# Kernel tuning notes

Hardware: AMD Instinct MI355X
Metric: run time of the kernel (lower is better)

The kernel has to match this reference:

```python
import jax, jax.numpy as jnp
import numpy as np

GAMMA = 1.0 / 512.0  # RBF bandwidth, 1/d_feat


def _rbf_kernel(X, Z, gamma):
    # X: [N, d], Z: [M, d] -> K: [N, M], K[i,j] = exp(-gamma * ||x_i - z_j||^2)
    xn = jnp.sum(X * X, axis=1, keepdims=True)        # [N, 1]
    zn = jnp.sum(Z * Z, axis=1, keepdims=True).T      # [1, M]
    sq = xn + zn - 2.0 * (X @ Z.T)                    # [N, M]
    return jnp.exp(-gamma * jnp.maximum(sq, 0.0))


def setup_inputs() -> dict:
    key = jax.random.key(0)
    k1, k2, k3, k4, k5 = jax.random.split(key, 5)
    N, d, M = 8192, 512, 4096
    inputs = jax.random.normal(k1, (M, d), dtype=jnp.float32)
    X = jax.random.normal(k2, (N, d), dtype=jnp.float32)
    # SVM labels in {-1, +1}
    Y = jnp.where(jax.random.uniform(k3, (N, 1)) > 0.5, 1.0, -1.0).astype(jnp.float32)
    a = jax.random.normal(k4, (N, 1), dtype=jnp.float32) * 0.1
    b = jax.random.normal(k5, (1, 1), dtype=jnp.float32)
    return {"inputs": inputs, "X": X, "Y": Y, "a": a, "b": b}


def reference(inputs, X, Y, a, b):
    # K: [N, M]; weighted sum over support vectors N, then add bias, transpose.
    K = _rbf_kernel(X, inputs, GAMMA)                 # [N, M]
    s = jnp.sum(a * Y * K, axis=0)                    # [M]
    out = (s + b)                                     # [1, M] via broadcast with [1,1]
    return out.T                                      # [M, 1]
```

## Files before the change

kernel.cpp:

```cpp
#include <hip/hip_runtime.h>
#include <hip/hip_bf16.h>
#include <stdint.h>

#define C2EXP (-0.0028179443441958f)

static constexpr int N_SV = 8192;
static constexpr int M_Q  = 4096;
static constexpr int DIM  = 512;
static constexpr int NP_A = N_SV / 16;
static constexpr int NP_B = M_Q / 16;
static constexpr int NKT  = DIM / 32;

typedef __bf16 bf16x8 __attribute__((ext_vector_type(8)));
typedef float  f32x4  __attribute__((ext_vector_type(4)));

#define GLB const __attribute__((address_space(1))) void
#define LDS __attribute__((address_space(3))) void

__global__ __launch_bounds__(256) void svm_prep(
    const float* __restrict__ Z, const float* __restrict__ X,
    const float* __restrict__ Y, const float* __restrict__ a,
    const float* __restrict__ b,
    __bf16* __restrict__ Xp, __bf16* __restrict__ Zp,
    float* __restrict__ xn, float* __restrict__ zn, float* __restrict__ w,
    float* __restrict__ out)
{
    __shared__ float part[4][16];

    const int tid  = threadIdx.x;
    const int lane = tid & 63;
    const int wv   = tid >> 6;
    const int pb   = blockIdx.x;
    const bool isA = (pb < NP_A);
    const int p    = isA ? pb : pb - NP_A;
    const float* src = (isA ? X : Z) + (size_t)p * 16 * DIM;
    __bf16* dst  = isA ? Xp : Zp;
    const int np = isA ? NP_A : NP_B;

    const int q    = p & 15;
    const int tile = p >> 4;
    const int slot = isA ? (((q >> 2) & 1) * 8 + (q >> 3) * 4 + (q & 3))
                         : (((q >> 1) & 1) * 8 + (q >> 2) * 2 + (q & 1));
    const size_t stIdx = (size_t)tile * 16 + slot;

    const int row = lane & 15;
    const int ch  = lane >> 4;

    float s = 0.0f;
    #pragma unroll
    for (int f = 0; f < 4; ++f) {
        const int kt = wv * 4 + f;
        const float4* rp = (const float4*)(src + (size_t)row * DIM + kt * 32 + ch * 8);
        float4 v0 = rp[0], v1 = rp[1];
        s += v0.x*v0.x + v0.y*v0.y + v0.z*v0.z + v0.w*v0.w
           + v1.x*v1.x + v1.y*v1.y + v1.z*v1.z + v1.w*v1.w;
        __bf16 h[8] = {(__bf16)v0.x, (__bf16)v0.y, (__bf16)v0.z, (__bf16)v0.w,
                       (__bf16)v1.x, (__bf16)v1.y, (__bf16)v1.z, (__bf16)v1.w};
        uint4 bits;
        __builtin_memcpy(&bits, h, 16);
        *(uint4*)((char*)dst + (((size_t)kt * np + stIdx) << 10) + lane * 16) = bits;
    }

    s += __shfl_xor(s, 16);
    s += __shfl_xor(s, 32);
    if (lane < 16) part[wv][lane] = s;
    __syncthreads();

    if (tid < 16) {
        const float t = part[0][tid] + part[1][tid] + part[2][tid] + part[3][tid];
        const int r = p * 16 + tid;
        if (isA) { xn[r] = t; w[r] = a[r] * Y[r]; }
        else     { zn[r] = t; out[r] = b[0]; }
    }
}

__global__ __launch_bounds__(512, 2) void svm_main(
    const __bf16* __restrict__ Xp, const __bf16* __restrict__ Zp,
    const float* __restrict__ xn, const float* __restrict__ zn,
    const float* __restrict__ w, float* __restrict__ out)
{
    __shared__ char Sh[65536];

    const int tid  = threadIdx.x;
    const int lane = tid & 63;
    const int wid  = tid >> 6;
    const int wr   = wid >> 2;
    const int wc   = wid & 3;

    const int iBase = blockIdx.y * 256;
    const int jBase = blockIdx.x * 256;
    const int pbA   = blockIdx.y * 16;
    const int pbB   = blockIdx.x * 16;

    f32x4 acc[8][4];
    #pragma unroll
    for (int m = 0; m < 8; ++m)
        #pragma unroll
        for (int n = 0; n < 4; ++n)
            acc[m][n] = (f32x4)(0.0f);

    auto stageH = [&](const __bf16* Mp, int pb16, int kt, int op, int h, int np) {
        char* dst = (char*)Sh + (kt & 1) * 32768 + op * 16384 + h * 8192 + tid * 16;
        const char* s0 = (const char*)Mp + (((size_t)kt * np + pb16) << 10)
                       + h * 8192 + tid * 16;
        __builtin_amdgcn_global_load_lds((GLB*)s0, (LDS*)dst, 16, 0, 0);
    };

    stageH(Xp, pbA, 0, 0, 0, NP_A);
    stageH(Xp, pbA, 0, 0, 1, NP_A);
    stageH(Zp, pbB, 0, 1, 0, NP_B);
    stageH(Zp, pbB, 0, 1, 1, NP_B);
    stageH(Xp, pbA, 1, 0, 0, NP_A);
    stageH(Xp, pbA, 1, 0, 1, NP_A);
    stageH(Zp, pbB, 1, 1, 0, NP_B);
    stageH(Zp, pbB, 1, 1, 1, NP_B);
    asm volatile("s_waitcnt vmcnt(4)" ::: "memory");
    __builtin_amdgcn_s_barrier();

    bf16x8 af[4], bf[4];

    #pragma unroll
    for (int t = 0; t < NKT; ++t) {
        const int buf = t & 1;
        const char* Ab = (const char*)Sh + buf * 32768 + lane * 16;
        const char* Bb = Ab + 16384;

        #pragma unroll
        for (int mi = 0; mi < 4; ++mi)
            af[mi] = *(const bf16x8*)(Ab + (wr * 4 + mi) * 1024);
        #pragma unroll
        for (int j = 0; j < 2; ++j)
            bf[j] = *(const bf16x8*)(Bb + (wc * 2 + j) * 1024);
        __builtin_amdgcn_s_barrier();
        asm volatile("s_waitcnt lgkmcnt(0)" ::: "memory");
        __builtin_amdgcn_sched_barrier(0);
        __builtin_amdgcn_s_setprio(1);
        #pragma unroll
        for (int mi = 0; mi < 4; ++mi)
            #pragma unroll
            for (int n = 0; n < 2; ++n)
                acc[mi][n] = __builtin_amdgcn_mfma_f32_16x16x32_bf16(
                    af[mi], bf[n], acc[mi][n], 0, 0, 0);
        __builtin_amdgcn_s_setprio(0);
        __builtin_amdgcn_s_barrier();

        #pragma unroll
        for (int j = 0; j < 2; ++j)
            bf[2 + j] = *(const bf16x8*)(Bb + (8 + wc * 2 + j) * 1024);
        if (t + 2 < NKT) {
            stageH(Xp, pbA, t + 2, 0, 0, NP_A);
            stageH(Zp, pbB, t + 2, 1, 0, NP_B);
        }
        __builtin_amdgcn_s_barrier();
        asm volatile("s_waitcnt lgkmcnt(0)" ::: "memory");
        __builtin_amdgcn_sched_barrier(0);
        __builtin_amdgcn_s_setprio(1);
        #pragma unroll
        for (int mi = 0; mi < 4; ++mi)
            #pragma unroll
            for (int n = 2; n < 4; ++n)
                acc[mi][n] = __builtin_amdgcn_mfma_f32_16x16x32_bf16(
                    af[mi], bf[n], acc[mi][n], 0, 0, 0);
        __builtin_amdgcn_s_setprio(0);
        __builtin_amdgcn_s_barrier();

        #pragma unroll
        for (int mi = 0; mi < 4; ++mi)
            af[mi] = *(const bf16x8*)(Ab + (8 + wr * 4 + mi) * 1024);
        if (t + 2 < NKT)
            stageH(Zp, pbB, t + 2, 1, 1, NP_B);
        __builtin_amdgcn_s_barrier();
        asm volatile("s_waitcnt lgkmcnt(0)" ::: "memory");
        __builtin_amdgcn_sched_barrier(0);
        __builtin_amdgcn_s_setprio(1);
        #pragma unroll
        for (int mi = 0; mi < 4; ++mi)
            #pragma unroll
            for (int n = 0; n < 2; ++n)
                acc[4 + mi][n] = __builtin_amdgcn_mfma_f32_16x16x32_bf16(
                    af[mi], bf[n], acc[4 + mi][n], 0, 0, 0);
        __builtin_amdgcn_s_setprio(0);
        __builtin_amdgcn_s_barrier();

        if (t + 2 < NKT)
            stageH(Xp, pbA, t + 2, 0, 1, NP_A);
        __builtin_amdgcn_s_barrier();
        asm volatile("s_waitcnt lgkmcnt(0)" ::: "memory");
        __builtin_amdgcn_sched_barrier(0);
        __builtin_amdgcn_s_setprio(1);
        #pragma unroll
        for (int mi = 0; mi < 4; ++mi)
            #pragma unroll
            for (int n = 2; n < 4; ++n)
                acc[4 + mi][n] = __builtin_amdgcn_mfma_f32_16x16x32_bf16(
                    af[mi], bf[n], acc[4 + mi][n], 0, 0, 0);
        __builtin_amdgcn_s_setprio(0);
        if (t < NKT - 2) {
            asm volatile("s_waitcnt vmcnt(4)" ::: "memory");
        } else if (t == NKT - 2) {
            asm volatile("s_waitcnt vmcnt(0)" ::: "memory");
        }
        __builtin_amdgcn_s_barrier();
    }

    const int rg   = lane >> 4;
    const int lcol = lane & 15;

    float znv[4];
    #pragma unroll
    for (int n = 0; n < 4; ++n)
        znv[n] = zn[jBase + wc * 64 + n * 16 + lcol];

    float cs[4] = {0.f, 0.f, 0.f, 0.f};
    #pragma unroll
    for (int m = 0; m < 8; ++m) {
        float wv[4], xv[4];
        #pragma unroll
        for (int r = 0; r < 4; ++r) {
            const int i = iBase + wr * 128 + m * 16 + rg * 4 + r;
            wv[r] = w[i];
            xv[r] = xn[i];
        }
        #pragma unroll
        for (int n = 0; n < 4; ++n)
            #pragma unroll
            for (int r = 0; r < 4; ++r) {
                float d = xv[r] + znv[n] - 2.0f * acc[m][n][r];
                d = fmaxf(d, 0.0f);
                cs[n] += wv[r] * exp2f(C2EXP * d);
            }
    }

    #pragma unroll
    for (int n = 0; n < 4; ++n) {
        const int j = jBase + wc * 64 + n * 16 + lcol;
        float c = cs[n];
        c += __shfl_xor(c, 16);
        c += __shfl_xor(c, 32);
        if (lane < 16) atomicAdd(out + j, c);
    }
}

extern "C" void kernel_launch(void* const* d_in, const int* in_sizes, int n_in,
                              void* d_out, int out_size, void* d_ws, size_t ws_size,
                              hipStream_t stream)
{
    const float* Z = (const float*)d_in[0];
    const float* X = (const float*)d_in[1];
    const float* Y = (const float*)d_in[2];
    const float* a = (const float*)d_in[3];
    const float* b = (const float*)d_in[4];
    float* out = (float*)d_out;

    char* ws = (char*)d_ws;
    __bf16* Xp = (__bf16*)ws;
    __bf16* Zp = (__bf16*)(ws + 8ull * 1024 * 1024);
    float*  xn = (float*)(ws + 12ull * 1024 * 1024);
    float*  zn = xn + N_SV;
    float*  w  = zn + M_Q;

    svm_prep<<<NP_A + NP_B, 256, 0, stream>>>(Z, X, Y, a, b, Xp, Zp, xn, zn, w, out);
    svm_main<<<dim3(M_Q / 256, N_SV / 256), 512, 0, stream>>>(Xp, Zp, xn, zn, w, out);
}
```

Measured before the change: 113.5 us.

## Restructure GEMM main loop into two phases with fewer barriers

Rewrites the K-loop schedule of the fused RBF GEMM. Each iteration now has two 16-MFMA phases instead of four 8-MFMA phases. The global-to-LDS staging is split into a one-load part issued one tile ahead and a three-load part issued two tiles ahead, with vmcnt waits adjusted to match. The goal is to cut barrier and waitcnt stalls per K-step and give each phase more MFMA work. In exchange, B fragments are held in more registers at once, and the reworked prefetch and wait ordering raises the risk of LDS races.

```diff
diff --git a/kernel.cpp b/kernel.cpp
--- a/kernel.cpp
+++ b/kernel.cpp
@@ -105,15 +105,18 @@
                        + h * 8192 + tid * 16;
         __builtin_amdgcn_global_load_lds((GLB*)s0, (LDS*)dst, 16, 0, 0);
     };
-
-    stageH(Xp, pbA, 0, 0, 0, NP_A);
-    stageH(Xp, pbA, 0, 0, 1, NP_A);
-    stageH(Zp, pbB, 0, 1, 0, NP_B);
-    stageH(Zp, pbB, 0, 1, 1, NP_B);
-    stageH(Xp, pbA, 1, 0, 0, NP_A);
-    stageH(Xp, pbA, 1, 0, 1, NP_A);
-    stageH(Zp, pbB, 1, 1, 0, NP_B);
-    stageH(Zp, pbB, 1, 1, 1, NP_B);
+    auto stage3 = [&](int kt) {
+        stageH(Xp, pbA, kt, 0, 0, NP_A);
+        stageH(Zp, pbB, kt, 1, 0, NP_B);
+        stageH(Zp, pbB, kt, 1, 1, NP_B);
+    };
+    auto stage1 = [&](int kt) {
+        stageH(Xp, pbA, kt, 0, 1, NP_A);
+    };
+
+    stage3(0);
+    stage1(0);
+    stage3(1);
     asm volatile("s_waitcnt vmcnt(4)" ::: "memory");
     __builtin_amdgcn_s_barrier();
 
@@ -121,86 +124,51 @@
 
     #pragma unroll
     for (int t = 0; t < NKT; ++t) {
-        const int buf = t & 1;
-        const char* Ab = (const char*)Sh + buf * 32768 + lane * 16;
+        const char* Ab = (const char*)Sh + (t & 1) * 32768 + lane * 16;
         const char* Bb = Ab + 16384;
 
+        if (t + 1 < NKT) stage1(t + 1);
         #pragma unroll
         for (int mi = 0; mi < 4; ++mi)
             af[mi] = *(const bf16x8*)(Ab + (wr * 4 + mi) * 1024);
         #pragma unroll
-        for (int j = 0; j < 2; ++j)
-            bf[j] = *(const bf16x8*)(Bb + (wc * 2 + j) * 1024);
+        for (int j = 0; j < 2; ++j) {
+            bf[j]     = *(const bf16x8*)(Bb + (wc * 2 + j) * 1024);
+            bf[2 + j] = *(const bf16x8*)(Bb + (8 + wc * 2 + j) * 1024);
+        }
+        asm volatile("s_waitcnt lgkmcnt(0)" ::: "memory");
+        if (t < NKT - 1) { asm volatile("s_waitcnt vmcnt(4)" ::: "memory"); }
+        else             { asm volatile("s_waitcnt vmcnt(0)" ::: "memory"); }
         __builtin_amdgcn_s_barrier();
-        asm volatile("s_waitcnt lgkmcnt(0)" ::: "memory");
-        __builtin_amdgcn_sched_barrier(0);
         __builtin_amdgcn_s_setprio(1);
         #pragma unroll
         for (int mi = 0; mi < 4; ++mi)
             #pragma unroll
-            for (int n = 0; n < 2; ++n)
+            for (int n = 0; n < 4; ++n)
                 acc[mi][n] = __builtin_amdgcn_mfma_f32_16x16x32_bf16(
                     af[mi], bf[n], acc[mi][n], 0, 0, 0);
         __builtin_amdgcn_s_setprio(0);
-        __builtin_amdgcn_s_barrier();
-
-        #pragma unroll
-        for (int j = 0; j < 2; ++j)
-            bf[2 + j] = *(const bf16x8*)(Bb + (8 + wc * 2 + j) * 1024);
-        if (t + 2 < NKT) {
-            stageH(Xp, pbA, t + 2, 0, 0, NP_A);
-            stageH(Zp, pbB, t + 2, 1, 0, NP_B);
+
+        if (t + 2 < NKT) stage3(t + 2);
+        #pragma unroll
+        for (int mi = 0; mi < 4; ++mi)
+            af[mi] = *(const bf16x8*)(Ab + (8 + wr * 4 + mi) * 1024);
+        asm volatile("s_waitcnt lgkmcnt(0)" ::: "memory");
+        if (t < NKT - 2) {
+            asm volatile("s_waitcnt vmcnt(4)" ::: "memory");
+            __builtin_amdgcn_s_barrier();
+        } else if (t == NKT - 2) {
+            asm volatile("s_waitcnt vmcnt(1)" ::: "memory");
+            __builtin_amdgcn_s_barrier();
         }
-        __builtin_amdgcn_s_barrier();
-        asm volatile("s_waitcnt lgkmcnt(0)" ::: "memory");
-        __builtin_amdgcn_sched_barrier(0);
         __builtin_amdgcn_s_setprio(1);
         #pragma unroll
         for (int mi = 0; mi < 4; ++mi)
             #pragma unroll
-            for (int n = 2; n < 4; ++n)
-                acc[mi][n] = __builtin_amdgcn_mfma_f32_16x16x32_bf16(
-                    af[mi], bf[n], acc[mi][n], 0, 0, 0);
-        __builtin_amdgcn_s_setprio(0);
-        __builtin_amdgcn_s_barrier();
-
-        #pragma unroll
-        for (int mi = 0; mi < 4; ++mi)
-            af[mi] = *(const bf16x8*)(Ab + (8 + wr * 4 + mi) * 1024);
-        if (t + 2 < NKT)
-            stageH(Zp, pbB, t + 2, 1, 1, NP_B);
-        __builtin_amdgcn_s_barrier();
-        asm volatile("s_waitcnt lgkmcnt(0)" ::: "memory");
-        __builtin_amdgcn_sched_barrier(0);
-        __builtin_amdgcn_s_setprio(1);
-        #pragma unroll
-        for (int mi = 0; mi < 4; ++mi)
-            #pragma unroll
-            for (int n = 0; n < 2; ++n)
+            for (int n = 0; n < 4; ++n)
                 acc[4 + mi][n] = __builtin_amdgcn_mfma_f32_16x16x32_bf16(
                     af[mi], bf[n], acc[4 + mi][n], 0, 0, 0);
         __builtin_amdgcn_s_setprio(0);
-        __builtin_amdgcn_s_barrier();
-
-        if (t + 2 < NKT)
-            stageH(Xp, pbA, t + 2, 0, 1, NP_A);
-        __builtin_amdgcn_s_barrier();
-        asm volatile("s_waitcnt lgkmcnt(0)" ::: "memory");
-        __builtin_amdgcn_sched_barrier(0);
-        __builtin_amdgcn_s_setprio(1);
-        #pragma unroll
-        for (int mi = 0; mi < 4; ++mi)
-            #pragma unroll
-            for (int n = 2; n < 4; ++n)
-                acc[4 + mi][n] = __builtin_amdgcn_mfma_f32_16x16x32_bf16(
-                    af[mi], bf[n], acc[4 + mi][n], 0, 0, 0);
-        __builtin_amdgcn_s_setprio(0);
-        if (t < NKT - 2) {
-            asm volatile("s_waitcnt vmcnt(4)" ::: "memory");
-        } else if (t == NKT - 2) {
-            asm volatile("s_waitcnt vmcnt(0)" ::: "memory");
-        }
-        __builtin_amdgcn_s_barrier();
     }
 
     const int rg   = lane >> 4;
```

Result: no change. 111.5 us (-1.7%).
